# Kernel optimization log

Measured on AMD Instinct MI355X. Metric: run time of the kernel, lower is better.

Reference implementation:

```python
import jax, jax.numpy as jnp
import numpy as np

KSIZE = 13
DIL = 3
NUM_HEADS = 4
LN_EPS = 1e-5


def _na_idx(L, k, d):
    # NATTEN-style dilated neighborhood indices along one axis.
    i = jnp.arange(L)
    g, ii = i % d, i // d                       # dilation group, index within group
    Lg = (L - g + d - 1) // d                   # group length per position
    start = jnp.clip(ii - k // 2, 0, Lg - k)    # clamped window start (group coords)
    offs = jnp.arange(k)
    nbr = g[:, None] + d * (start[:, None] + offs[None, :])           # (L,k) absolute idx
    rel = start[:, None] + offs[None, :] - ii[:, None] + (k - 1)      # (L,k) rpb index in [0,2k-2]
    return nbr, rel


def _layernorm(x, g, b):
    mu = jnp.mean(x, -1, keepdims=True)
    var = jnp.mean(jnp.square(x - mu), -1, keepdims=True)
    return (x - mu) * jax.lax.rsqrt(var + LN_EPS) * g + b


def setup_inputs() -> dict:
    key = jax.random.key(0)
    ks = jax.random.split(key, 12)
    B, H, W, C = 1, 96, 96, 64
    mh = int(C * 4.0)
    s = 0.02
    return {
        "x": jax.random.normal(ks[0], (B, H * W, C), jnp.float32),
        "norm1_g": jnp.ones((C,), jnp.float32),
        "norm1_b": jnp.zeros((C,), jnp.float32),
        "qkv_w": jax.random.normal(ks[1], (C, 3 * C), jnp.float32) * s,
        "qkv_b": jnp.zeros((3 * C,), jnp.float32),
        "rpb": jax.random.normal(ks[2], (NUM_HEADS, 2 * KSIZE - 1, 2 * KSIZE - 1), jnp.float32) * s,
        "proj_w": jax.random.normal(ks[3], (C, C), jnp.float32) * s,
        "proj_b": jnp.zeros((C,), jnp.float32),
        "norm2_g": jnp.ones((C,), jnp.float32),
        "norm2_b": jnp.zeros((C,), jnp.float32),
        "fc1_w": jax.random.normal(ks[4], (C, mh), jnp.float32) * s,
        "fc1_b": jnp.zeros((mh,), jnp.float32),
        "fc2_w": jax.random.normal(ks[5], (mh, C), jnp.float32) * s,
        "fc2_b": jnp.zeros((C,), jnp.float32),
        "H": H,
        "W": W,
    }


def _ga(h, qkv_w, qkv_b, rpb, proj_w, proj_b):
    # h: (B,H,W,C) -> dilated neighborhood attention, kernel=13, dilation=3
    B, H, W, C = h.shape
    nh, hd = NUM_HEADS, C // NUM_HEADS
    scale = hd ** -0.5
    qkv = (h @ qkv_w + qkv_b).reshape(B, H, W, 3, nh, hd)
    qkv = qkv.transpose(3, 0, 4, 1, 2, 5)       # (3,B,nh,H,W,hd)
    q, k, v = qkv[0] * scale, qkv[1], qkv[2]
    idx_h, rel_h = _na_idx(H, KSIZE, DIL)
    idx_w, rel_w = _na_idx(W, KSIZE, DIL)
    Kk = KSIZE

    def gather(t):  # (B,nh,H,W,hd) -> (B,nh,H,W,Kk*Kk,hd)
        t = jnp.take(t, idx_h, axis=2)          # (B,nh,H,Kk,W,hd)
        t = jnp.take(t, idx_w, axis=4)          # (B,nh,H,Kk,W,Kk,hd)
        return t.transpose(0, 1, 2, 4, 3, 5, 6).reshape(B, nh, H, W, Kk * Kk, hd)

    kg = gather(k)
    vg = gather(v)
    logits = jnp.einsum('bnhwc,bnhwkc->bnhwk', q, kg)
    bias = rpb[:, rel_h]                         # (nh,H,Kk,2K-1)
    bias = bias[:, :, :, rel_w]                  # (nh,H,Kk,W,Kk)
    bias = bias.transpose(0, 1, 3, 2, 4).reshape(nh, H, W, Kk * Kk)
    attn = jax.nn.softmax(logits + bias[None], axis=-1)
    out = jnp.einsum('bnhwk,bnhwkc->bnhwc', attn, vg)
    out = out.transpose(0, 2, 3, 1, 4).reshape(B, H, W, C)
    return out @ proj_w + proj_b


def reference(x, norm1_g, norm1_b, qkv_w, qkv_b, rpb, proj_w, proj_b,
              norm2_g, norm2_b, fc1_w, fc1_b, fc2_w, fc2_b, H, W):
    B, N, C = x.shape
    shortcut = x
    h = _layernorm(x, norm1_g, norm1_b).reshape(B, H, W, C)
    h = _ga(h, qkv_w, qkv_b, rpb, proj_w, proj_b).reshape(B, N, C)
    x = shortcut + h
    h2 = _layernorm(x, norm2_g, norm2_b)
    mlp = jax.nn.gelu(h2 @ fc1_w + fc1_b, approximate=False) @ fc2_w + fc2_b
    return x + mlp
```

## Files before the change

### kernel.cpp

```cpp
#include <hip/hip_runtime.h>
#include <math.h>

#define HH 96
#define WW 96
#define CC 64
#define NH 4
#define HD 16
#define KS 13
#define KK (KS*KS)
#define NTOK (HH*WW)

template<int CTRL>
__device__ __forceinline__ float dpp_add(float p) {
    int t = __builtin_amdgcn_update_dpp(0, __float_as_int(p), CTRL, 0xF, 0xF, true);
    return p + __int_as_float(t);
}

__device__ __forceinline__ float dpp_reduce8(float p) {
    p = dpp_add<0xB1>(p);
    p = dpp_add<0x4E>(p);
    p = dpp_add<0x141>(p);
    return p;
}

__device__ __forceinline__ void ln_rows32(float (*buf)[34],
                                          const float* __restrict__ g,
                                          const float* __restrict__ b,
                                          int tid) {
    int r  = tid >> 3;
    int c0 = (tid & 7) * 8;
    float v[8];
    float s = 0.0f;
    #pragma unroll
    for (int j = 0; j < 8; j++) { v[j] = buf[c0 + j][r]; s += v[j]; }
    s = dpp_reduce8(s);
    float mu = s * (1.0f / 64.0f);
    float s2 = 0.0f;
    #pragma unroll
    for (int j = 0; j < 8; j++) { float d = v[j] - mu; s2 += d * d; }
    s2 = dpp_reduce8(s2);
    float inv = rsqrtf(s2 * (1.0f / 64.0f) + 1e-5f);
    #pragma unroll
    for (int j = 0; j < 8; j++)
        buf[c0 + j][r] = (v[j] - mu) * inv * g[c0 + j] + b[c0 + j];
}

__global__ __launch_bounds__(256) void ln_gemm_kernel(const float* __restrict__ x,
                                                      const float* __restrict__ g,
                                                      const float* __restrict__ b,
                                                      const float* __restrict__ W,
                                                      const float* __restrict__ bias,
                                                      float* __restrict__ out) {
    __shared__ float Ast[64][34];
    const int t0 = blockIdx.x * 32;
    const int tid = threadIdx.x;

    for (int i = tid; i < 32 * 64; i += 256) {
        int r = i >> 6, cc = i & 63;
        Ast[cc][r] = x[t0 * 64 + i];
    }
    __syncthreads();
    ln_rows32(Ast, g, b, tid);
    __syncthreads();

    const int tc = tid & 15;
    const int tr = tid >> 4;
    const int r0 = tr * 2;
    const int c  = blockIdx.y * 64 + tc * 4;

    float4 b4 = *(const float4*)&bias[c];
    float4 acc0 = b4, acc1 = b4;
    #pragma unroll 8
    for (int k = 0; k < 64; k++) {
        float2 a = *(const float2*)&Ast[k][r0];
        float4 w = *(const float4*)&W[k * 192 + c];
        acc0.x += a.x * w.x; acc0.y += a.x * w.y; acc0.z += a.x * w.z; acc0.w += a.x * w.w;
        acc1.x += a.y * w.x; acc1.y += a.y * w.y; acc1.z += a.y * w.z; acc1.w += a.y * w.w;
    }
    if (blockIdx.y == 0) {
        acc0.x *= 0.25f; acc0.y *= 0.25f; acc0.z *= 0.25f; acc0.w *= 0.25f;
        acc1.x *= 0.25f; acc1.y *= 0.25f; acc1.z *= 0.25f; acc1.w *= 0.25f;
    }
    *(float4*)&out[(t0 + r0) * 192 + c] = acc0;
    *(float4*)&out[(t0 + r0 + 1) * 192 + c] = acc1;
}

__global__ __launch_bounds__(256) void na_attn_kernel(const float* __restrict__ qkv,
                                                      const float* __restrict__ rpb,
                                                      float* __restrict__ out) {
    int wave = threadIdx.x >> 6;
    int lane = threadIdx.x & 63;
    int bid  = blockIdx.x;
    int swz  = (bid & 7) * 288 + (bid >> 3);
    int y    = swz / 24;
    int rem  = swz - y * 24;
    int gw   = rem >> 3;
    int iw   = (rem & 7) * 4 + wave;
    int token = y * WW + gw + 3 * iw;

    int head = lane >> 4;
    int slot = (lane >> 2) & 3;
    int l    = lane & 3;
    int co   = head * HD + l * 4;

    int gh = y % 3, ih = y / 3;
    int sh = ih - 6; sh = sh < 0 ? 0 : (sh > 19 ? 19 : sh);
    int sw = iw - 6; sw = sw < 0 ? 0 : (sw > 19 ? 19 : sw);

    float4 q4 = *(const float4*)&qkv[token * 192 + co];
    const float* bias_h = rpb + head * 625 + (sw - iw + 12);

    const int xpart = (gw + 3 * sw) * 192 + 64 + co + slot * 576;

    float4 acc = make_float4(0.f, 0.f, 0.f, 0.f);
    float s = 0.0f;

    for (int kh = 0; kh < KS; kh++) {
        int ny = gh + 3 * (sh + kh);
        const float* kp = qkv + ny * (WW * 192) + xpart;
        const float* bp = bias_h + (sh + kh - ih + 12) * 25;
        #pragma unroll
        for (int i = 0; i < 3; i++) {
            float4 k4 = *(const float4*)(kp + i * 2304);
            float4 v4 = *(const float4*)(kp + i * 2304 + 64);
            float p = q4.x * k4.x + q4.y * k4.y + q4.z * k4.z + q4.w * k4.w;
            p = dpp_add<0xB1>(p);
            p = dpp_add<0x4E>(p);
            float e = __expf(p + bp[4 * i + slot]);
            s += e;
            acc.x += e * v4.x; acc.y += e * v4.y; acc.z += e * v4.z; acc.w += e * v4.w;
        }
        if (slot == 0) {
            float4 k4 = *(const float4*)(kp + 3 * 2304);
            float4 v4 = *(const float4*)(kp + 3 * 2304 + 64);
            float p = q4.x * k4.x + q4.y * k4.y + q4.z * k4.z + q4.w * k4.w;
            p = dpp_add<0xB1>(p);
            p = dpp_add<0x4E>(p);
            float e = __expf(p + bp[12]);
            s += e;
            acc.x += e * v4.x; acc.y += e * v4.y; acc.z += e * v4.z; acc.w += e * v4.w;
        }
    }

    s = dpp_add<0x128>(s);  s = dpp_add<0x124>(s);
    acc.x = dpp_add<0x128>(acc.x); acc.x = dpp_add<0x124>(acc.x);
    acc.y = dpp_add<0x128>(acc.y); acc.y = dpp_add<0x124>(acc.y);
    acc.z = dpp_add<0x128>(acc.z); acc.z = dpp_add<0x124>(acc.z);
    acc.w = dpp_add<0x128>(acc.w); acc.w = dpp_add<0x124>(acc.w);

    if (slot == 0) {
        float inv = 1.0f / s;
        *(float4*)&out[token * CC + co] =
            make_float4(acc.x * inv, acc.y * inv, acc.z * inv, acc.w * inv);
    }
}

__global__ __launch_bounds__(256) void mlp_fused_kernel(const float* __restrict__ attn_out,
                                                        const float* __restrict__ x,
                                                        const float* __restrict__ proj_w,
                                                        const float* __restrict__ proj_b,
                                                        const float* __restrict__ n2g,
                                                        const float* __restrict__ n2b,
                                                        const float* __restrict__ fc1_w,
                                                        const float* __restrict__ fc1_b,
                                                        const float* __restrict__ fc2_w,
                                                        const float* __restrict__ fc2_b,
                                                        float* __restrict__ out) {
    __shared__ float Ast[64][34];
    __shared__ float X2T[64][34];
    __shared__ float Hid[256][34];

    const int t0 = blockIdx.x * 32;
    const int tid = threadIdx.x;

    for (int i = tid; i < 32 * 64; i += 256) {
        int r = i >> 6, cc = i & 63;
        Ast[cc][r] = attn_out[t0 * 64 + i];
    }
    __syncthreads();

    const int tc = tid & 15;
    const int tr = tid >> 4;
    const int r0 = tr * 2;
    const int c  = tc * 4;

    float4 pb = *(const float4*)&proj_b[c];
    float4 a0 = pb, a1 = pb;
    #pragma unroll 8
    for (int k = 0; k < 64; k++) {
        float2 a = *(const float2*)&Ast[k][r0];
        float4 w = *(const float4*)&proj_w[k * 64 + c];
        a0.x += a.x * w.x; a0.y += a.x * w.y; a0.z += a.x * w.z; a0.w += a.x * w.w;
        a1.x += a.y * w.x; a1.y += a.y * w.y; a1.z += a.y * w.z; a1.w += a.y * w.w;
    }
    {
        float4 x0 = *(const float4*)&x[(t0 + r0) * 64 + c];
        float4 x1 = *(const float4*)&x[(t0 + r0 + 1) * 64 + c];
        a0.x += x0.x; a0.y += x0.y; a0.z += x0.z; a0.w += x0.w;
        a1.x += x1.x; a1.y += x1.y; a1.z += x1.z; a1.w += x1.w;
    }
    X2T[c + 0][r0] = a0.x; X2T[c + 1][r0] = a0.y; X2T[c + 2][r0] = a0.z; X2T[c + 3][r0] = a0.w;
    X2T[c + 0][r0 + 1] = a1.x; X2T[c + 1][r0 + 1] = a1.y; X2T[c + 2][r0 + 1] = a1.z; X2T[c + 3][r0 + 1] = a1.w;
    __syncthreads();

    ln_rows32(X2T, n2g, n2b, tid);
    __syncthreads();

    float4 h0[4], h1[4];
    #pragma unroll
    for (int gg = 0; gg < 4; gg++) {
        float4 bb = *(const float4*)&fc1_b[c + gg * 64];
        h0[gg] = bb; h1[gg] = bb;
    }
    #pragma unroll 4
    for (int k = 0; k < 64; k++) {
        float2 a = *(const float2*)&X2T[k][r0];
        #pragma unroll
        for (int gg = 0; gg < 4; gg++) {
            float4 w = *(const float4*)&fc1_w[k * 256 + c + gg * 64];
            h0[gg].x += a.x * w.x; h0[gg].y += a.x * w.y; h0[gg].z += a.x * w.z; h0[gg].w += a.x * w.w;
            h1[gg].x += a.y * w.x; h1[gg].y += a.y * w.y; h1[gg].z += a.y * w.z; h1[gg].w += a.y * w.w;
        }
    }
    #define GELU1(v) v = 0.5f * v * (1.0f + erff(v * 0.70710678118f))
    #pragma unroll
    for (int gg = 0; gg < 4; gg++) {
        GELU1(h0[gg].x); GELU1(h0[gg].y); GELU1(h0[gg].z); GELU1(h0[gg].w);
        GELU1(h1[gg].x); GELU1(h1[gg].y); GELU1(h1[gg].z); GELU1(h1[gg].w);
    }
    #undef GELU1
    #pragma unroll
    for (int gg = 0; gg < 4; gg++) {
        int col = c + gg * 64;
        Hid[col + 0][r0] = h0[gg].x; Hid[col + 1][r0] = h0[gg].y;
        Hid[col + 2][r0] = h0[gg].z; Hid[col + 3][r0] = h0[gg].w;
        Hid[col + 0][r0 + 1] = h1[gg].x; Hid[col + 1][r0 + 1] = h1[gg].y;
        Hid[col + 2][r0 + 1] = h1[gg].z; Hid[col + 3][r0 + 1] = h1[gg].w;
    }
    __syncthreads();

    float4 ob = *(const float4*)&fc2_b[c];
    float4 o0 = ob, o1 = ob;
    #pragma unroll 8
    for (int k = 0; k < 256; k++) {
        float2 a = *(const float2*)&Hid[k][r0];
        float4 w = *(const float4*)&fc2_w[k * 64 + c];
        o0.x += a.x * w.x; o0.y += a.x * w.y; o0.z += a.x * w.z; o0.w += a.x * w.w;
        o1.x += a.y * w.x; o1.y += a.y * w.y; o1.z += a.y * w.z; o1.w += a.y * w.w;
    }
    o0.x += a0.x; o0.y += a0.y; o0.z += a0.z; o0.w += a0.w;
    o1.x += a1.x; o1.y += a1.y; o1.z += a1.z; o1.w += a1.w;
    *(float4*)&out[(t0 + r0) * 64 + c] = o0;
    *(float4*)&out[(t0 + r0 + 1) * 64 + c] = o1;
}

extern "C" void kernel_launch(void* const* d_in, const int* in_sizes, int n_in,
                              void* d_out, int out_size, void* d_ws, size_t ws_size,
                              hipStream_t stream) {
    const float* x       = (const float*)d_in[0];
    const float* norm1_g = (const float*)d_in[1];
    const float* norm1_b = (const float*)d_in[2];
    const float* qkv_w   = (const float*)d_in[3];
    const float* qkv_b   = (const float*)d_in[4];
    const float* rpb     = (const float*)d_in[5];
    const float* proj_w  = (const float*)d_in[6];
    const float* proj_b  = (const float*)d_in[7];
    const float* norm2_g = (const float*)d_in[8];
    const float* norm2_b = (const float*)d_in[9];
    const float* fc1_w   = (const float*)d_in[10];
    const float* fc1_b   = (const float*)d_in[11];
    const float* fc2_w   = (const float*)d_in[12];
    const float* fc2_b   = (const float*)d_in[13];
    float* out = (float*)d_out;

    float* ws = (float*)d_ws;
    float* qkv      = ws;
    float* attn_out = qkv + NTOK * 192;

    dim3 blk(256);
    ln_gemm_kernel<<<dim3(NTOK / 32, 3), blk, 0, stream>>>(x, norm1_g, norm1_b, qkv_w, qkv_b, qkv);
    na_attn_kernel<<<NTOK / 4, blk, 0, stream>>>(qkv, rpb, attn_out);
    mlp_fused_kernel<<<NTOK / 32, blk, 0, stream>>>(attn_out, x, proj_w, proj_b,
                                                    norm2_g, norm2_b, fc1_w, fc1_b,
                                                    fc2_w, fc2_b, out);
}
```

Baseline: 170.9 us.

## Shrink MLP fused kernel tile to 8 tokens per block for more blocks

The fused proj+LN2+MLP kernel now processes 8 tokens per 256-thread block instead of 32, with each thread computing a 1x2 output tile rather than 2x4. This gives four times as many blocks (1152) to fill the GPU's compute units and cuts shared memory per block. The cost is less register-level reuse: each weight load now feeds fewer FMAs, so total global/L2 weight traffic per token rises by a factor of four. LayerNorm is reworked to use 128 threads with a 16-lane DPP reduction.

```diff
diff --git a/kernel.cpp b/kernel.cpp
--- a/kernel.cpp
+++ b/kernel.cpp
@@ -20,6 +20,11 @@
     p = dpp_add<0xB1>(p);
     p = dpp_add<0x4E>(p);
     p = dpp_add<0x141>(p);
+    return p;
+}
+__device__ __forceinline__ float dpp_reduce16(float p) {
+    p = dpp_reduce8(p);
+    p = dpp_add<0x140>(p);
     return p;
 }
 
@@ -166,92 +171,92 @@
                                                         const float* __restrict__ fc2_w,
                                                         const float* __restrict__ fc2_b,
                                                         float* __restrict__ out) {
-    __shared__ float Ast[64][34];
-    __shared__ float X2T[64][34];
-    __shared__ float Hid[256][34];
-
-    const int t0 = blockIdx.x * 32;
+    __shared__ float Ast[64][9];
+    __shared__ float X2T[64][9];
+    __shared__ float Hid[256][9];
+
+    const int t0 = blockIdx.x * 8;
     const int tid = threadIdx.x;
-
-    for (int i = tid; i < 32 * 64; i += 256) {
+    const int tc = tid & 31;
+    const int tr = tid >> 5;
+    const int c2 = tc * 2;
+
+    {
+        float2 v = *(const float2*)&attn_out[t0 * 64 + tid * 2];
+        int i = tid * 2;
         int r = i >> 6, cc = i & 63;
-        Ast[cc][r] = attn_out[t0 * 64 + i];
-    }
-    __syncthreads();
-
-    const int tc = tid & 15;
-    const int tr = tid >> 4;
-    const int r0 = tr * 2;
-    const int c  = tc * 4;
-
-    float4 pb = *(const float4*)&proj_b[c];
-    float4 a0 = pb, a1 = pb;
+        Ast[cc][r] = v.x;
+        Ast[cc + 1][r] = v.y;
+    }
+    __syncthreads();
+
+    float2 a0 = *(const float2*)&proj_b[c2];
     #pragma unroll 8
     for (int k = 0; k < 64; k++) {
-        float2 a = *(const float2*)&Ast[k][r0];
-        float4 w = *(const float4*)&proj_w[k * 64 + c];
-        a0.x += a.x * w.x; a0.y += a.x * w.y; a0.z += a.x * w.z; a0.w += a.x * w.w;
-        a1.x += a.y * w.x; a1.y += a.y * w.y; a1.z += a.y * w.z; a1.w += a.y * w.w;
+        float a = Ast[k][tr];
+        float2 w = *(const float2*)&proj_w[k * 64 + c2];
+        a0.x += a * w.x; a0.y += a * w.y;
     }
     {
-        float4 x0 = *(const float4*)&x[(t0 + r0) * 64 + c];
-        float4 x1 = *(const float4*)&x[(t0 + r0 + 1) * 64 + c];
-        a0.x += x0.x; a0.y += x0.y; a0.z += x0.z; a0.w += x0.w;
-        a1.x += x1.x; a1.y += x1.y; a1.z += x1.z; a1.w += x1.w;
-    }
-    X2T[c + 0][r0] = a0.x; X2T[c + 1][r0] = a0.y; X2T[c + 2][r0] = a0.z; X2T[c + 3][r0] = a0.w;
-    X2T[c + 0][r0 + 1] = a1.x; X2T[c + 1][r0 + 1] = a1.y; X2T[c + 2][r0 + 1] = a1.z; X2T[c + 3][r0 + 1] = a1.w;
-    __syncthreads();
-
-    ln_rows32(X2T, n2g, n2b, tid);
-    __syncthreads();
-
-    float4 h0[4], h1[4];
-    #pragma unroll
-    for (int gg = 0; gg < 4; gg++) {
-        float4 bb = *(const float4*)&fc1_b[c + gg * 64];
-        h0[gg] = bb; h1[gg] = bb;
-    }
+        float2 xr = *(const float2*)&x[(t0 + tr) * 64 + c2];
+        a0.x += xr.x; a0.y += xr.y;
+    }
+    X2T[c2][tr] = a0.x; X2T[c2 + 1][tr] = a0.y;
+    __syncthreads();
+
+    if (tid < 128) {
+        int r  = tid >> 4;
+        int c0 = (tid & 15) * 4;
+        float v[4];
+        float s = 0.0f;
+        #pragma unroll
+        for (int j = 0; j < 4; j++) { v[j] = X2T[c0 + j][r]; s += v[j]; }
+        s = dpp_reduce16(s);
+        float mu = s * (1.0f / 64.0f);
+        float s2 = 0.0f;
+        #pragma unroll
+        for (int j = 0; j < 4; j++) { float d = v[j] - mu; s2 += d * d; }
+        s2 = dpp_reduce16(s2);
+        float inv = rsqrtf(s2 * (1.0f / 64.0f) + 1e-5f);
+        #pragma unroll
+        for (int j = 0; j < 4; j++)
+            X2T[c0 + j][r] = (v[j] - mu) * inv * n2g[c0 + j] + n2b[c0 + j];
+    }
+    __syncthreads();
+
+    float2 h[4];
+    #pragma unroll
+    for (int gg = 0; gg < 4; gg++)
+        h[gg] = *(const float2*)&fc1_b[c2 + gg * 64];
     #pragma unroll 4
     for (int k = 0; k < 64; k++) {
-        float2 a = *(const float2*)&X2T[k][r0];
+        float a = X2T[k][tr];
         #pragma unroll
         for (int gg = 0; gg < 4; gg++) {
-            float4 w = *(const float4*)&fc1_w[k * 256 + c + gg * 64];
-            h0[gg].x += a.x * w.x; h0[gg].y += a.x * w.y; h0[gg].z += a.x * w.z; h0[gg].w += a.x * w.w;
-            h1[gg].x += a.y * w.x; h1[gg].y += a.y * w.y; h1[gg].z += a.y * w.z; h1[gg].w += a.y * w.w;
+            float2 w = *(const float2*)&fc1_w[k * 256 + c2 + gg * 64];
+            h[gg].x += a * w.x; h[gg].y += a * w.y;
         }
     }
     #define GELU1(v) v = 0.5f * v * (1.0f + erff(v * 0.70710678118f))
     #pragma unroll
+    for (int gg = 0; gg < 4; gg++) { GELU1(h[gg].x); GELU1(h[gg].y); }
+    #undef GELU1
+    #pragma unroll
     for (int gg = 0; gg < 4; gg++) {
-        GELU1(h0[gg].x); GELU1(h0[gg].y); GELU1(h0[gg].z); GELU1(h0[gg].w);
-        GELU1(h1[gg].x); GELU1(h1[gg].y); GELU1(h1[gg].z); GELU1(h1[gg].w);
-    }
-    #undef GELU1
-    #pragma unroll
-    for (int gg = 0; gg < 4; gg++) {
-        int col = c + gg * 64;
-        Hid[col + 0][r0] = h0[gg].x; Hid[col + 1][r0] = h0[gg].y;
-        Hid[col + 2][r0] = h0[gg].z; Hid[col + 3][r0] = h0[gg].w;
-        Hid[col + 0][r0 + 1] = h1[gg].x; Hid[col + 1][r0 + 1] = h1[gg].y;
-        Hid[col + 2][r0 + 1] = h1[gg].z; Hid[col + 3][r0 + 1] = h1[gg].w;
-    }
-    __syncthreads();
-
-    float4 ob = *(const float4*)&fc2_b[c];
-    float4 o0 = ob, o1 = ob;
+        Hid[c2 + gg * 64][tr]     = h[gg].x;
+        Hid[c2 + 1 + gg * 64][tr] = h[gg].y;
+    }
+    __syncthreads();
+
+    float2 o = *(const float2*)&fc2_b[c2];
     #pragma unroll 8
     for (int k = 0; k < 256; k++) {
-        float2 a = *(const float2*)&Hid[k][r0];
-        float4 w = *(const float4*)&fc2_w[k * 64 + c];
-        o0.x += a.x * w.x; o0.y += a.x * w.y; o0.z += a.x * w.z; o0.w += a.x * w.w;
-        o1.x += a.y * w.x; o1.y += a.y * w.y; o1.z += a.y * w.z; o1.w += a.y * w.w;
-    }
-    o0.x += a0.x; o0.y += a0.y; o0.z += a0.z; o0.w += a0.w;
-    o1.x += a1.x; o1.y += a1.y; o1.z += a1.z; o1.w += a1.w;
-    *(float4*)&out[(t0 + r0) * 64 + c] = o0;
-    *(float4*)&out[(t0 + r0 + 1) * 64 + c] = o1;
+        float a = Hid[k][tr];
+        float2 w = *(const float2*)&fc2_w[k * 64 + c2];
+        o.x += a * w.x; o.y += a * w.y;
+    }
+    o.x += a0.x; o.y += a0.y;
+    *(float2*)&out[(t0 + tr) * 64 + c2] = o;
 }
 
 extern "C" void kernel_launch(void* const* d_in, const int* in_sizes, int n_in,
@@ -280,7 +285,7 @@
     dim3 blk(256);
     ln_gemm_kernel<<<dim3(NTOK / 32, 3), blk, 0, stream>>>(x, norm1_g, norm1_b, qkv_w, qkv_b, qkv);
     na_attn_kernel<<<NTOK / 4, blk, 0, stream>>>(qkv, rpb, attn_out);
-    mlp_fused_kernel<<<NTOK / 32, blk, 0, stream>>>(attn_out, x, proj_w, proj_b,
-                                                    norm2_g, norm2_b, fc1_w, fc1_b,
-                                                    fc2_w, fc2_b, out);
-}
+    mlp_fused_kernel<<<NTOK / 8, blk, 0, stream>>>(attn_out, x, proj_w, proj_b,
+                                                   norm2_g, norm2_b, fc1_w, fc1_b,
+                                                   fc2_w, fc2_b, out);
+}
```

Result: slower. 219.1 us (+28.2%).

## Use 4x4 register tiles with 128-thread blocks in fused MLP kernel

Applied to the files above, without the earlier changes.

The fused proj+LN2+MLP kernel now runs 128 threads per block, with each thread computing a 4-row by 4-column register tile instead of 2x4. Shared-memory tiles are padded to 36 so rows can be read and written as float4. LayerNorm is done inline with a 4-lane DPP reduction, and the input is loaded as float4. The aim is more reuse of each weight load per thread and fewer LDS instructions, at the cost of more registers and half as many threads per block. A leftover loop writes dummy values into Hid before they are overwritten, which adds redundant LDS stores.

```diff
diff --git a/kernel.cpp b/kernel.cpp
--- a/kernel.cpp
+++ b/kernel.cpp
@@ -155,7 +155,7 @@
     }
 }
 
-__global__ __launch_bounds__(256) void mlp_fused_kernel(const float* __restrict__ attn_out,
+__global__ __launch_bounds__(128) void mlp_fused_kernel(const float* __restrict__ attn_out,
                                                         const float* __restrict__ x,
                                                         const float* __restrict__ proj_w,
                                                         const float* __restrict__ proj_b,
@@ -166,92 +166,137 @@
                                                         const float* __restrict__ fc2_w,
                                                         const float* __restrict__ fc2_b,
                                                         float* __restrict__ out) {
-    __shared__ float Ast[64][34];
-    __shared__ float X2T[64][34];
-    __shared__ float Hid[256][34];
+    __shared__ float Ast[64][36];
+    __shared__ float X2T[64][36];
+    __shared__ float Hid[256][36];
 
     const int t0 = blockIdx.x * 32;
     const int tid = threadIdx.x;
-
-    for (int i = tid; i < 32 * 64; i += 256) {
-        int r = i >> 6, cc = i & 63;
-        Ast[cc][r] = attn_out[t0 * 64 + i];
-    }
-    __syncthreads();
-
     const int tc = tid & 15;
     const int tr = tid >> 4;
-    const int r0 = tr * 2;
+    const int r0 = tr * 4;
     const int c  = tc * 4;
 
+    #pragma unroll
+    for (int j = 0; j < 4; j++) {
+        int idx = tid + 128 * j;
+        float4 v = ((const float4*)attn_out)[t0 * 16 + idx];
+        int row = idx >> 4, cc = (idx & 15) * 4;
+        Ast[cc][row] = v.x; Ast[cc + 1][row] = v.y;
+        Ast[cc + 2][row] = v.z; Ast[cc + 3][row] = v.w;
+    }
+    __syncthreads();
+
     float4 pb = *(const float4*)&proj_b[c];
-    float4 a0 = pb, a1 = pb;
+    float4 a[4] = {pb, pb, pb, pb};
     #pragma unroll 8
     for (int k = 0; k < 64; k++) {
-        float2 a = *(const float2*)&Ast[k][r0];
+        float4 aa = *(const float4*)&Ast[k][r0];
+        float  ar[4] = {aa.x, aa.y, aa.z, aa.w};
         float4 w = *(const float4*)&proj_w[k * 64 + c];
-        a0.x += a.x * w.x; a0.y += a.x * w.y; a0.z += a.x * w.z; a0.w += a.x * w.w;
-        a1.x += a.y * w.x; a1.y += a.y * w.y; a1.z += a.y * w.z; a1.w += a.y * w.w;
-    }
+        #pragma unroll
+        for (int i = 0; i < 4; i++) {
+            a[i].x += ar[i] * w.x; a[i].y += ar[i] * w.y;
+            a[i].z += ar[i] * w.z; a[i].w += ar[i] * w.w;
+        }
+    }
+    #pragma unroll
+    for (int i = 0; i < 4; i++) {
+        float4 xr = *(const float4*)&x[(t0 + r0 + i) * 64 + c];
+        a[i].x += xr.x; a[i].y += xr.y; a[i].z += xr.z; a[i].w += xr.w;
+        X2T[c][r0 + i] = a[i].x; X2T[c + 1][r0 + i] = a[i].y;
+        X2T[c + 2][r0 + i] = a[i].z; X2T[c + 3][r0 + i] = a[i].w;
+    }
+    __syncthreads();
+
     {
-        float4 x0 = *(const float4*)&x[(t0 + r0) * 64 + c];
-        float4 x1 = *(const float4*)&x[(t0 + r0 + 1) * 64 + c];
-        a0.x += x0.x; a0.y += x0.y; a0.z += x0.z; a0.w += x0.w;
-        a1.x += x1.x; a1.y += x1.y; a1.z += x1.z; a1.w += x1.w;
-    }
-    X2T[c + 0][r0] = a0.x; X2T[c + 1][r0] = a0.y; X2T[c + 2][r0] = a0.z; X2T[c + 3][r0] = a0.w;
-    X2T[c + 0][r0 + 1] = a1.x; X2T[c + 1][r0 + 1] = a1.y; X2T[c + 2][r0 + 1] = a1.z; X2T[c + 3][r0 + 1] = a1.w;
-    __syncthreads();
-
-    ln_rows32(X2T, n2g, n2b, tid);
-    __syncthreads();
-
-    float4 h0[4], h1[4];
+        int r  = tid >> 2;
+        int c0 = (tid & 3) * 16;
+        float v[16];
+        float s = 0.0f;
+        #pragma unroll
+        for (int j = 0; j < 16; j++) { v[j] = X2T[c0 + j][r]; s += v[j]; }
+        s = dpp_add<0xB1>(s); s = dpp_add<0x4E>(s);
+        float mu = s * (1.0f / 64.0f);
+        float s2 = 0.0f;
+        #pragma unroll
+        for (int j = 0; j < 16; j++) { float d = v[j] - mu; s2 += d * d; }
+        s2 = dpp_add<0xB1>(s2); s2 = dpp_add<0x4E>(s2);
+        float inv = rsqrtf(s2 * (1.0f / 64.0f) + 1e-5f);
+        #pragma unroll
+        for (int j = 0; j < 16; j++)
+            X2T[c0 + j][r] = (v[j] - mu) * inv * n2g[c0 + j] + n2b[c0 + j];
+    }
+    __syncthreads();
+
+    float4 h[4][4];
     #pragma unroll
     for (int gg = 0; gg < 4; gg++) {
         float4 bb = *(const float4*)&fc1_b[c + gg * 64];
-        h0[gg] = bb; h1[gg] = bb;
+        #pragma unroll
+        for (int i = 0; i < 4; i++) h[i][gg] = bb;
     }
     #pragma unroll 4
     for (int k = 0; k < 64; k++) {
-        float2 a = *(const float2*)&X2T[k][r0];
+        float4 aa = *(const float4*)&X2T[k][r0];
+        float  ar[4] = {aa.x, aa.y, aa.z, aa.w};
         #pragma unroll
         for (int gg = 0; gg < 4; gg++) {
             float4 w = *(const float4*)&fc1_w[k * 256 + c + gg * 64];
-            h0[gg].x += a.x * w.x; h0[gg].y += a.x * w.y; h0[gg].z += a.x * w.z; h0[gg].w += a.x * w.w;
-            h1[gg].x += a.y * w.x; h1[gg].y += a.y * w.y; h1[gg].z += a.y * w.z; h1[gg].w += a.y * w.w;
+            #pragma unroll
+            for (int i = 0; i < 4; i++) {
+                h[i][gg].x += ar[i] * w.x; h[i][gg].y += ar[i] * w.y;
+                h[i][gg].z += ar[i] * w.z; h[i][gg].w += ar[i] * w.w;
+            }
         }
     }
     #define GELU1(v) v = 0.5f * v * (1.0f + erff(v * 0.70710678118f))
     #pragma unroll
+    for (int i = 0; i < 4; i++)
+        #pragma unroll
+        for (int gg = 0; gg < 4; gg++) {
+            GELU1(h[i][gg].x); GELU1(h[i][gg].y); GELU1(h[i][gg].z); GELU1(h[i][gg].w);
+        }
+    #undef GELU1
+    #pragma unroll
     for (int gg = 0; gg < 4; gg++) {
-        GELU1(h0[gg].x); GELU1(h0[gg].y); GELU1(h0[gg].z); GELU1(h0[gg].w);
-        GELU1(h1[gg].x); GELU1(h1[gg].y); GELU1(h1[gg].z); GELU1(h1[gg].w);
-    }
-    #undef GELU1
+        #pragma unroll
+        for (int j = 0; j < 4; j++) {
+            *(float4*)&Hid[c + gg * 64 + j][r0] =
+                make_float4(h[0][gg + 0].x, 0.f, 0.f, 0.f);
+        }
+    }
     #pragma unroll
     for (int gg = 0; gg < 4; gg++) {
-        int col = c + gg * 64;
-        Hid[col + 0][r0] = h0[gg].x; Hid[col + 1][r0] = h0[gg].y;
-        Hid[col + 2][r0] = h0[gg].z; Hid[col + 3][r0] = h0[gg].w;
-        Hid[col + 0][r0 + 1] = h1[gg].x; Hid[col + 1][r0 + 1] = h1[gg].y;
-        Hid[col + 2][r0 + 1] = h1[gg].z; Hid[col + 3][r0 + 1] = h1[gg].w;
+        float4 col0 = make_float4(h[0][gg].x, h[1][gg].x, h[2][gg].x, h[3][gg].x);
+        float4 col1 = make_float4(h[0][gg].y, h[1][gg].y, h[2][gg].y, h[3][gg].y);
+        float4 col2 = make_float4(h[0][gg].z, h[1][gg].z, h[2][gg].z, h[3][gg].z);
+        float4 col3 = make_float4(h[0][gg].w, h[1][gg].w, h[2][gg].w, h[3][gg].w);
+        *(float4*)&Hid[c + gg * 64 + 0][r0] = col0;
+        *(float4*)&Hid[c + gg * 64 + 1][r0] = col1;
+        *(float4*)&Hid[c + gg * 64 + 2][r0] = col2;
+        *(float4*)&Hid[c + gg * 64 + 3][r0] = col3;
     }
     __syncthreads();
 
     float4 ob = *(const float4*)&fc2_b[c];
-    float4 o0 = ob, o1 = ob;
+    float4 o[4] = {ob, ob, ob, ob};
     #pragma unroll 8
     for (int k = 0; k < 256; k++) {
-        float2 a = *(const float2*)&Hid[k][r0];
+        float4 aa = *(const float4*)&Hid[k][r0];
+        float  ar[4] = {aa.x, aa.y, aa.z, aa.w};
         float4 w = *(const float4*)&fc2_w[k * 64 + c];
-        o0.x += a.x * w.x; o0.y += a.x * w.y; o0.z += a.x * w.z; o0.w += a.x * w.w;
-        o1.x += a.y * w.x; o1.y += a.y * w.y; o1.z += a.y * w.z; o1.w += a.y * w.w;
-    }
-    o0.x += a0.x; o0.y += a0.y; o0.z += a0.z; o0.w += a0.w;
-    o1.x += a1.x; o1.y += a1.y; o1.z += a1.z; o1.w += a1.w;
-    *(float4*)&out[(t0 + r0) * 64 + c] = o0;
-    *(float4*)&out[(t0 + r0 + 1) * 64 + c] = o1;
+        #pragma unroll
+        for (int i = 0; i < 4; i++) {
+            o[i].x += ar[i] * w.x; o[i].y += ar[i] * w.y;
+            o[i].z += ar[i] * w.z; o[i].w += ar[i] * w.w;
+        }
+    }
+    #pragma unroll
+    for (int i = 0; i < 4; i++) {
+        o[i].x += a[i].x; o[i].y += a[i].y; o[i].z += a[i].z; o[i].w += a[i].w;
+        *(float4*)&out[(t0 + r0 + i) * 64 + c] = o[i];
+    }
 }
 
 extern "C" void kernel_launch(void* const* d_in, const int* in_sizes, int n_in,
@@ -280,7 +325,7 @@
     dim3 blk(256);
     ln_gemm_kernel<<<dim3(NTOK / 32, 3), blk, 0, stream>>>(x, norm1_g, norm1_b, qkv_w, qkv_b, qkv);
     na_attn_kernel<<<NTOK / 4, blk, 0, stream>>>(qkv, rpb, attn_out);
-    mlp_fused_kernel<<<NTOK / 32, blk, 0, stream>>>(attn_out, x, proj_w, proj_b,
-                                                    norm2_g, norm2_b, fc1_w, fc1_b,
-                                                    fc2_w, fc2_b, out);
-}
+    mlp_fused_kernel<<<NTOK / 32, dim3(128), 0, stream>>>(attn_out, x, proj_w, proj_b,
+                                                          norm2_g, norm2_b, fc1_w, fc1_b,
+                                                          fc2_w, fc2_b, out);
+}
```

After: 164.5 us. 3.8% less time.
